# Optimization experiments

Hardware: AMD Instinct MI355X
Metric: run time of the kernel (lower is better)

The kernel has to match this reference:

```python
import jax, jax.numpy as jnp
import numpy as np

N = 50000       # num_node
E = 800000      # num edges (avg degree 32)
F_IN, F_HID, F_OUT = 128, 128, 64


def setup_inputs() -> dict:
    key = jax.random.key(0)
    ks = jax.random.split(key, 8)
    x = jax.random.normal(ks[0], (N, F_IN), dtype=jnp.float32)
    edge_index = jax.random.randint(ks[1], (2, E), 0, N, dtype=jnp.int64)
    edge_weight = jax.random.uniform(ks[2], (E,), dtype=jnp.float32)
    s1 = 1.0 / np.sqrt(F_IN)
    s2 = 1.0 / np.sqrt(F_HID)
    W1 = jax.random.normal(ks[3], (F_HID, F_IN), dtype=jnp.float32) * s1
    b1 = jnp.zeros((F_HID,), dtype=jnp.float32)
    W2 = jax.random.normal(ks[4], (F_HID, F_HID), dtype=jnp.float32) * s2
    b2 = jnp.zeros((F_HID,), dtype=jnp.float32)
    W3 = jax.random.normal(ks[5], (F_OUT, F_HID), dtype=jnp.float32) * s2
    b3 = jnp.zeros((F_OUT,), dtype=jnp.float32)
    return {"x": x, "edge_index": edge_index, "edge_weight": edge_weight,
            "W1": W1, "b1": b1, "W2": W2, "b2": b2, "W3": W3, "b3": b3}


def _gcn_norm(edge_index, edge_weight, num_nodes):
    # PyG gcn_norm: add self-loops (weight 1), symmetric D^-1/2 (A+I) D^-1/2
    loop = jnp.arange(num_nodes, dtype=edge_index.dtype)
    row = jnp.concatenate([edge_index[0], loop])  # source
    col = jnp.concatenate([edge_index[1], loop])  # target (aggregation index)
    ew = jnp.concatenate([edge_weight, jnp.ones((num_nodes,), edge_weight.dtype)])
    deg = jax.ops.segment_sum(ew, col, num_segments=num_nodes)
    deg_safe = jnp.where(deg > 0, deg, 1.0)
    dinv = jnp.where(deg > 0, jax.lax.rsqrt(deg_safe), 0.0)
    norm = dinv[row] * ew * dinv[col]  # [E+N]
    return row, col, norm


def reference(x, edge_index, edge_weight, W1, b1, W2, b2, W3, b3):
    num_nodes = x.shape[0]
    row, col, norm = _gcn_norm(edge_index, edge_weight, num_nodes)
    h = x
    for W, b in ((W1, b1), (W2, b2), (W3, b3)):
        m = h @ W.T                                   # [N, d_out]
        msg = m[row] * norm[:, None]                  # gather + scale, [E+N, d_out]
        agg = jax.ops.segment_sum(msg, col, num_segments=num_nodes)
        h = jax.nn.relu(agg + b)                      # GCNConv bias then ReLU
    return h.reshape(-1)                              # torch.flatten
```

## Files before the change

### kernel.cpp

```cpp
#include <hip/hip_runtime.h>
#include <hip/hip_fp16.h>


#define K_DIM 128
#define SORT_ITEMS 2048

typedef unsigned long long u64;
typedef unsigned int u32;

using half8   = __attribute__((ext_vector_type(8))) _Float16;
using floatx4 = __attribute__((ext_vector_type(4))) float;


__global__ void build_kernel(const int* __restrict__ row, const int* __restrict__ col,
                             const float* __restrict__ ew, u64* __restrict__ el,
                             int E, int N) {
    int i = blockIdx.x * blockDim.x + threadIdx.x;
    if (i < E) {
        el[i] = ((u64)(u32)col[i] << 48) | ((u64)(u32)row[i] << 32)
              | (u64)__float_as_uint(ew[i]);
    } else if (i < E + N) {
        int v = i - E;
        el[i] = ((u64)(u32)v << 48) | ((u64)(u32)v << 32)
              | (u64)__float_as_uint(1.0f);
    }
}

__global__ void p1_hist(const u64* __restrict__ el, u32* __restrict__ ghist,
                        int total, int nb) {
    __shared__ u32 bin[256];
    bin[threadIdx.x] = 0;
    __syncthreads();
    const int base = blockIdx.x * SORT_ITEMS;
    const int end = min(base + SORT_ITEMS, total);
    for (int i = base + threadIdx.x; i < end; i += 256)
        atomicAdd(&bin[(u32)(el[i] >> 56)], 1u);
    __syncthreads();
    ghist[(size_t)threadIdx.x * nb + blockIdx.x] = bin[threadIdx.x];
}

__global__ void digit_sum(const u32* __restrict__ ghist, u32* __restrict__ dsum, int nb) {
    __shared__ u32 s[256];
    const int d = blockIdx.x;
    u32 acc = 0;
    for (int i = threadIdx.x; i < nb; i += 256) acc += ghist[(size_t)d * nb + i];
    s[threadIdx.x] = acc;
    __syncthreads();
    for (int off = 128; off > 0; off >>= 1) {
        if (threadIdx.x < off) s[threadIdx.x] += s[threadIdx.x + off];
        __syncthreads();
    }
    if (threadIdx.x == 0) dsum[d] = s[0];
}

__global__ void dsum_scan(const u32* __restrict__ dsum, u32* __restrict__ dbase) {
    __shared__ u32 s[256];
    const int t = threadIdx.x;
    const u32 v = dsum[t];
    s[t] = v;
    __syncthreads();
    for (int off = 1; off < 256; off <<= 1) {
        u32 u = (t >= off) ? s[t - off] : 0;
        __syncthreads();
        s[t] += u;
        __syncthreads();
    }
    dbase[t] = s[t] - v;
    if (t == 255) dbase[256] = s[255];
}

__global__ void digit_scan(u32* __restrict__ ghist, const u32* __restrict__ dbase, int nb) {
    __shared__ u32 s[256];
    const int d = blockIdx.x, t = threadIdx.x;
    u32 carry = dbase[d];
    for (int base = 0; base < nb; base += 256) {
        const int i = base + t;
        const u32 v = (i < nb) ? ghist[(size_t)d * nb + i] : 0;
        s[t] = v;
        __syncthreads();
        for (int off = 1; off < 256; off <<= 1) {
            u32 u = (t >= off) ? s[t - off] : 0;
            __syncthreads();
            s[t] += u;
            __syncthreads();
        }
        if (i < nb) ghist[(size_t)d * nb + i] = carry + s[t] - v;
        carry += s[255];
        __syncthreads();
    }
}

__global__ void p1_scatter(const u64* __restrict__ el, const u32* __restrict__ ghist,
                           u64* __restrict__ out, int total, int nb) {
    __shared__ u32 cur[256];
    cur[threadIdx.x] = ghist[(size_t)threadIdx.x * nb + blockIdx.x];
    __syncthreads();
    const int base = blockIdx.x * SORT_ITEMS;
    const int end = min(base + SORT_ITEMS, total);
    for (int i = base + threadIdx.x; i < end; i += 256) {
        u64 e = el[i];
        u32 p = atomicAdd(&cur[(u32)(e >> 56)], 1u);
        out[p] = e;
    }
}

__global__ void p2_sort(const u64* __restrict__ in, u64* __restrict__ out,
                        const u32* __restrict__ dbase) {
    const int t = threadIdx.x;
    const int base = (int)dbase[blockIdx.x];
    const int size = (int)dbase[blockIdx.x + 1] - base;
    __shared__ u32 hist[256], cur[256], s[256];
    hist[t] = 0;
    __syncthreads();
    for (int i = t; i < size; i += 256)
        atomicAdd(&hist[(u32)(in[base + i] >> 48) & 0xFFu], 1u);
    __syncthreads();
    const u32 v = hist[t];
    s[t] = v;
    __syncthreads();
    for (int off = 1; off < 256; off <<= 1) {
        u32 u = (t >= off) ? s[t - off] : 0;
        __syncthreads();
        s[t] += u;
        __syncthreads();
    }
    cur[t] = (u32)base + s[t] - v;
    __syncthreads();
    for (int i = t; i < size; i += 256) {
        u64 e = in[base + i];
        u32 p = atomicAdd(&cur[(u32)(e >> 48) & 0xFFu], 1u);
        out[p] = e;
    }
}

__global__ void boundary_kernel(const u64* __restrict__ el, int* __restrict__ offs,
                                int total, int n) {
    int i = blockIdx.x * blockDim.x + threadIdx.x;
    if (i >= total) return;
    int c = (int)(el[i] >> 48);
    if (i == 0 || c != (int)(el[i - 1] >> 48)) offs[c] = i;
    if (i == 0) offs[n] = total;
}

__global__ void dinv_kernel(const u64* __restrict__ el, const int* __restrict__ offs,
                            float* __restrict__ dinv, int n) {
    int i = blockIdx.x * blockDim.x + threadIdx.x;
    if (i >= n) return;
    const int b = offs[i], e = offs[i + 1];
    float s = 0.f;
    for (int k = b; k < e; ++k)
        s += __uint_as_float((u32)(el[k] & 0xFFFFFFFFu));
    dinv[i] = rsqrtf(s);
}

__global__ void w2h_kernel(const float* __restrict__ W1, const float* __restrict__ W2,
                           const float* __restrict__ W3, __half* __restrict__ Wh,
                           int n1, int n2, int n3) {
    int i = blockIdx.x * blockDim.x + threadIdx.x;
    if (i >= n1 + n2 + n3) return;
    float v = (i < n1) ? W1[i] : (i < n1 + n2 ? W2[i - n1] : W3[i - n1 - n2]);
    Wh[i] = __float2half_rn(v);
}


template <int BN, bool FP32IN>
__global__ __launch_bounds__(256) void mfma_gemm(const void* __restrict__ Ain,
                                                 const __half* __restrict__ Wh,
                                                 const float* __restrict__ dinv,
                                                 __half* __restrict__ C, int nrows) {
    constexpr int NT = BN / 16;
    const int wave = threadIdx.x >> 6;
    const int lane = threadIdx.x & 63;
    const int quad = lane >> 4;
    const int l16  = lane & 15;
    const int row0 = blockIdx.x * 64 + wave * 16;

    int arow = row0 + l16;
    if (arow > nrows - 1) arow = nrows - 1;

    floatx4 acc[NT] = {};

#pragma unroll
    for (int kc = 0; kc < 4; ++kc) {
        const int kof = kc * 32 + quad * 8;
        half8 af;
        if constexpr (FP32IN) {
            const float* ap = (const float*)Ain + (size_t)arow * K_DIM + kof;
            float4 f0 = *(const float4*)ap;
            float4 f1 = *(const float4*)(ap + 4);
            af[0] = (_Float16)f0.x; af[1] = (_Float16)f0.y;
            af[2] = (_Float16)f0.z; af[3] = (_Float16)f0.w;
            af[4] = (_Float16)f1.x; af[5] = (_Float16)f1.y;
            af[6] = (_Float16)f1.z; af[7] = (_Float16)f1.w;
        } else {
            af = *(const half8*)((const __half*)Ain + (size_t)arow * K_DIM + kof);
        }
#pragma unroll
        for (int ct = 0; ct < NT; ++ct) {
            half8 bf = *(const half8*)(Wh + (size_t)(ct * 16 + l16) * K_DIM + kof);
            acc[ct] = __builtin_amdgcn_mfma_f32_16x16x32_f16(af, bf, acc[ct], 0, 0, 0);
        }
    }

    float dv[4];
    int grow[4];
    bool ok[4];
#pragma unroll
    for (int r = 0; r < 4; ++r) {
        grow[r] = row0 + quad * 4 + r;
        ok[r] = grow[r] < nrows;
        dv[r] = ok[r] ? dinv[grow[r]] : 0.f;
    }
#pragma unroll
    for (int ct = 0; ct < NT; ++ct) {
        const int colb = ct * 16 + l16;
#pragma unroll
        for (int r = 0; r < 4; ++r)
            if (ok[r])
                C[(size_t)grow[r] * BN + colb] = __float2half_rn(acc[ct][r] * dv[r]);
    }
}


template <int D, typename OUT>
__global__ __launch_bounds__(256) void agg_kernel(
    const __half* __restrict__ m, const int* __restrict__ offs,
    const int2* __restrict__ csr, const float* __restrict__ dinv,
    const float* __restrict__ bias, OUT* __restrict__ out, int n) {
    const int wid = threadIdx.x >> 6;
    const int lane = threadIdx.x & 63;
    const int node = (blockIdx.x << 2) + wid;
    if (node >= n) return;
    const int beg = offs[node];
    const int end = offs[node + 1];
    const __half2* mh = (const __half2*)m;
    float acc0 = 0.f, acc1 = 0.f;

    if constexpr (D == 128) {
        int k = beg;
        for (; k + 8 <= end; k += 8) {
            int2 e[8];
            float2 f[8];
#pragma unroll
            for (int j = 0; j < 8; ++j) e[j] = csr[k + j];
#pragma unroll
            for (int j = 0; j < 8; ++j)
                f[j] = __half22float2(mh[(size_t)(e[j].y & 0xFFFF) * 64 + lane]);
#pragma unroll
            for (int j = 0; j < 8; ++j) {
                float w = __int_as_float(e[j].x);
                acc0 = fmaf(w, f[j].x, acc0);
                acc1 = fmaf(w, f[j].y, acc1);
            }
        }
        for (; k < end; ++k) {
            int2 e0 = csr[k];
            float w0 = __int_as_float(e0.x);
            float2 f0 = __half22float2(mh[(size_t)(e0.y & 0xFFFF) * 64 + lane]);
            acc0 = fmaf(w0, f0.x, acc0); acc1 = fmaf(w0, f0.y, acc1);
        }
        const float dv = dinv[node];
        const float2 bv = *(const float2*)(bias + 2 * lane);
        float ox = fmaxf(acc0 * dv + bv.x, 0.f);
        float oy = fmaxf(acc1 * dv + bv.y, 0.f);
        if constexpr (sizeof(OUT) == 2) {
            ((__half2*)out)[(size_t)node * 64 + lane] = __floats2half2_rn(ox, oy);
        } else {
            *(float2*)((float*)out + (size_t)node * 128 + 2 * lane) = make_float2(ox, oy);
        }
    } else {
        const int half = lane >> 5;
        const int sl = lane & 31;
        int k = beg;
        for (; k + 8 <= end; k += 8) {
            int2 e0 = csr[k + half], e1 = csr[k + 2 + half];
            int2 e2 = csr[k + 4 + half], e3 = csr[k + 6 + half];
            float2 f0 = __half22float2(mh[(size_t)(e0.y & 0xFFFF) * 32 + sl]);
            float2 f1 = __half22float2(mh[(size_t)(e1.y & 0xFFFF) * 32 + sl]);
            float2 f2 = __half22float2(mh[(size_t)(e2.y & 0xFFFF) * 32 + sl]);
            float2 f3 = __half22float2(mh[(size_t)(e3.y & 0xFFFF) * 32 + sl]);
            float w0 = __int_as_float(e0.x), w1 = __int_as_float(e1.x);
            float w2 = __int_as_float(e2.x), w3 = __int_as_float(e3.x);
            acc0 = fmaf(w0, f0.x, acc0); acc1 = fmaf(w0, f0.y, acc1);
            acc0 = fmaf(w1, f1.x, acc0); acc1 = fmaf(w1, f1.y, acc1);
            acc0 = fmaf(w2, f2.x, acc0); acc1 = fmaf(w2, f2.y, acc1);
            acc0 = fmaf(w3, f3.x, acc0); acc1 = fmaf(w3, f3.y, acc1);
        }
        for (; k + 2 <= end; k += 2) {
            int2 e0 = csr[k + half];
            float w0 = __int_as_float(e0.x);
            float2 f0 = __half22float2(mh[(size_t)(e0.y & 0xFFFF) * 32 + sl]);
            acc0 = fmaf(w0, f0.x, acc0); acc1 = fmaf(w0, f0.y, acc1);
        }
        if (k < end && half == 0) {
            int2 e0 = csr[k];
            float w0 = __int_as_float(e0.x);
            float2 f0 = __half22float2(mh[(size_t)(e0.y & 0xFFFF) * 32 + sl]);
            acc0 = fmaf(w0, f0.x, acc0); acc1 = fmaf(w0, f0.y, acc1);
        }
        acc0 += __shfl_xor(acc0, 32);
        acc1 += __shfl_xor(acc1, 32);
        if (half == 0) {
            const float dv = dinv[node];
            const float2 bv = *(const float2*)(bias + 2 * sl);
            float ox = fmaxf(acc0 * dv + bv.x, 0.f);
            float oy = fmaxf(acc1 * dv + bv.y, 0.f);
            *(float2*)((float*)out + (size_t)node * 64 + 2 * sl) = make_float2(ox, oy);
        }
    }
}


extern "C" void kernel_launch(void* const* d_in, const int* in_sizes, int n_in,
                              void* d_out, int out_size, void* d_ws, size_t ws_size,
                              hipStream_t stream) {
    const float* x  = (const float*)d_in[0];
    const int*   ei = (const int*)d_in[1];
    const float* ew = (const float*)d_in[2];
    const float* W1 = (const float*)d_in[3];
    const float* b1 = (const float*)d_in[4];
    const float* W2 = (const float*)d_in[5];
    const float* b2 = (const float*)d_in[6];
    const float* W3 = (const float*)d_in[7];
    const float* b3 = (const float*)d_in[8];
    float* out = (float*)d_out;

    const int N = in_sizes[0] / K_DIM;
    const int E = in_sizes[2];
    const int* row = ei;
    const int* col = ei + E;

    const int total = E + N;
    const int nb = (total + SORT_ITEMS - 1) / SORT_ITEMS;
    const int ngroups = (N + 255) >> 8;
    const int NW1 = 128 * 128, NW2 = 128 * 128, NW3 = 64 * 128;

    u64* elA      = (u64*)d_ws;
    u64* elB      = elA + total;
    __half* m_buf = (__half*)(elB + total);
    __half* h_buf = m_buf + (size_t)N * K_DIM;
    __half* Wh    = h_buf + (size_t)N * K_DIM;
    u32* ghist    = (u32*)(Wh + NW1 + NW2 + NW3);
    u32* dsum     = ghist + (size_t)256 * nb;
    u32* dbase    = dsum + 256;
    int* offs     = (int*)(dbase + 257);
    float* dinv   = (float*)(offs + N + 1);

    build_kernel<<<(total + 255) / 256, 256, 0, stream>>>(row, col, ew, elA, E, N);
    p1_hist<<<nb, 256, 0, stream>>>(elA, ghist, total, nb);
    digit_sum<<<256, 256, 0, stream>>>(ghist, dsum, nb);
    dsum_scan<<<1, 256, 0, stream>>>(dsum, dbase);
    digit_scan<<<256, 256, 0, stream>>>(ghist, dbase, nb);
    p1_scatter<<<nb, 256, 0, stream>>>(elA, ghist, elB, total, nb);
    p2_sort<<<ngroups, 256, 0, stream>>>(elB, elA, dbase);
    boundary_kernel<<<(total + 255) / 256, 256, 0, stream>>>(elA, offs, total, N);
    dinv_kernel<<<(N + 255) / 256, 256, 0, stream>>>(elA, offs, dinv, N);
    w2h_kernel<<<(NW1 + NW2 + NW3 + 255) / 256, 256, 0, stream>>>(W1, W2, W3, Wh,
                                                                  NW1, NW2, NW3);

    const int gemm_blocks = (N + 63) / 64;
    const int agg_blocks = (N + 3) / 4;
    const int2* csr = (const int2*)elA;

    mfma_gemm<128, true><<<gemm_blocks, 256, 0, stream>>>(x, Wh, dinv, m_buf, N);
    agg_kernel<128, __half><<<agg_blocks, 256, 0, stream>>>(m_buf, offs, csr, dinv, b1, h_buf, N);
    mfma_gemm<128, false><<<gemm_blocks, 256, 0, stream>>>(h_buf, Wh + NW1, dinv, m_buf, N);
    agg_kernel<128, __half><<<agg_blocks, 256, 0, stream>>>(m_buf, offs, csr, dinv, b2, h_buf, N);
    mfma_gemm<64, false><<<gemm_blocks, 256, 0, stream>>>(h_buf, Wh + NW1 + NW2, dinv, m_buf, N);
    agg_kernel<64, float><<<agg_blocks, 256, 0, stream>>>(m_buf, offs, csr, dinv, b3, out, N);
}
```

Before: 313.4 us.

## Fuse CSR build preprocessing kernels to cut launches and global passes

Merges edge-list construction with the first radix histogram and folds the weight fp16 conversion into the same launch as extra blocks. The single-block digit-base scan is recomputed redundantly inside each digit_scan block. Segment offsets and degree rsqrt are now computed inside the second sort pass with shared-memory float atomics, removing the boundary and dinv kernels. This reduces kernel launches and extra reads of the sorted edge list. In exchange, the degree sums are accumulated in a nondeterministic order, and offsets are written only for nodes with nonzero count, which is always true here because of the self-loops.

```diff
diff --git a/kernel.cpp b/kernel.cpp
--- a/kernel.cpp
+++ b/kernel.cpp
@@ -12,31 +12,43 @@
 using floatx4 = __attribute__((ext_vector_type(4))) float;
 
 
-__global__ void build_kernel(const int* __restrict__ row, const int* __restrict__ col,
-                             const float* __restrict__ ew, u64* __restrict__ el,
-                             int E, int N) {
-    int i = blockIdx.x * blockDim.x + threadIdx.x;
-    if (i < E) {
-        el[i] = ((u64)(u32)col[i] << 48) | ((u64)(u32)row[i] << 32)
-              | (u64)__float_as_uint(ew[i]);
-    } else if (i < E + N) {
-        int v = i - E;
-        el[i] = ((u64)(u32)v << 48) | ((u64)(u32)v << 32)
-              | (u64)__float_as_uint(1.0f);
-    }
-}
-
-__global__ void p1_hist(const u64* __restrict__ el, u32* __restrict__ ghist,
-                        int total, int nb) {
+__global__ void build_hist(const int* __restrict__ row, const int* __restrict__ col,
+                           const float* __restrict__ ew, u64* __restrict__ el,
+                           u32* __restrict__ ghist, int E, int N, int nb,
+                           const float* __restrict__ W1, const float* __restrict__ W2,
+                           const float* __restrict__ W3, __half* __restrict__ Wh,
+                           int nw1, int nw2, int nw3) {
+    const int b = blockIdx.x;
+    if (b >= nb) {
+        const int i = (b - nb) * 256 + threadIdx.x;
+        const int tot = nw1 + nw2 + nw3;
+        if (i < tot) {
+            float v = (i < nw1) ? W1[i] : (i < nw1 + nw2 ? W2[i - nw1] : W3[i - nw1 - nw2]);
+            Wh[i] = __float2half_rn(v);
+        }
+        return;
+    }
     __shared__ u32 bin[256];
     bin[threadIdx.x] = 0;
     __syncthreads();
-    const int base = blockIdx.x * SORT_ITEMS;
+    const int total = E + N;
+    const int base = b * SORT_ITEMS;
     const int end = min(base + SORT_ITEMS, total);
-    for (int i = base + threadIdx.x; i < end; i += 256)
-        atomicAdd(&bin[(u32)(el[i] >> 56)], 1u);
-    __syncthreads();
-    ghist[(size_t)threadIdx.x * nb + blockIdx.x] = bin[threadIdx.x];
+    for (int i = base + threadIdx.x; i < end; i += 256) {
+        u64 e;
+        if (i < E) {
+            e = ((u64)(u32)col[i] << 48) | ((u64)(u32)row[i] << 32)
+              | (u64)__float_as_uint(ew[i]);
+        } else {
+            int v = i - E;
+            e = ((u64)(u32)v << 48) | ((u64)(u32)v << 32)
+              | (u64)__float_as_uint(1.0f);
+        }
+        el[i] = e;
+        atomicAdd(&bin[(u32)(e >> 56)], 1u);
+    }
+    __syncthreads();
+    ghist[(size_t)threadIdx.x * nb + b] = bin[threadIdx.x];
 }
 
 __global__ void digit_sum(const u32* __restrict__ ghist, u32* __restrict__ dsum, int nb) {
@@ -53,26 +65,22 @@
     if (threadIdx.x == 0) dsum[d] = s[0];
 }
 
-__global__ void dsum_scan(const u32* __restrict__ dsum, u32* __restrict__ dbase) {
-    __shared__ u32 s[256];
-    const int t = threadIdx.x;
-    const u32 v = dsum[t];
-    s[t] = v;
-    __syncthreads();
-    for (int off = 1; off < 256; off <<= 1) {
-        u32 u = (t >= off) ? s[t - off] : 0;
-        __syncthreads();
-        s[t] += u;
-        __syncthreads();
-    }
-    dbase[t] = s[t] - v;
-    if (t == 255) dbase[256] = s[255];
-}
-
-__global__ void digit_scan(u32* __restrict__ ghist, const u32* __restrict__ dbase, int nb) {
+__global__ void digit_scan(u32* __restrict__ ghist, const u32* __restrict__ dsum,
+                           u32* __restrict__ dbase, int nb) {
+    __shared__ u32 ds[256];
     __shared__ u32 s[256];
     const int d = blockIdx.x, t = threadIdx.x;
-    u32 carry = dbase[d];
+    ds[t] = dsum[t];
+    __syncthreads();
+    for (int off = 1; off < 256; off <<= 1) {
+        u32 u = (t >= off) ? ds[t - off] : 0;
+        __syncthreads();
+        ds[t] += u;
+        __syncthreads();
+    }
+    u32 carry = (d == 0) ? 0u : ds[d - 1];
+    if (t == 0) dbase[d] = carry;
+    if (d == 255 && t == 0) dbase[256] = ds[255];
     for (int base = 0; base < nb; base += 256) {
         const int i = base + t;
         const u32 v = (i < nb) ? ghist[(size_t)d * nb + i] : 0;
@@ -105,12 +113,15 @@
 }
 
 __global__ void p2_sort(const u64* __restrict__ in, u64* __restrict__ out,
-                        const u32* __restrict__ dbase) {
+                        const u32* __restrict__ dbase,
+                        int* __restrict__ offs, float* __restrict__ dinv, int n) {
     const int t = threadIdx.x;
     const int base = (int)dbase[blockIdx.x];
     const int size = (int)dbase[blockIdx.x + 1] - base;
     __shared__ u32 hist[256], cur[256], s[256];
+    __shared__ float wsum[256];
     hist[t] = 0;
+    wsum[t] = 0.f;
     __syncthreads();
     for (int i = t; i < size; i += 256)
         atomicAdd(&hist[(u32)(in[base + i] >> 48) & 0xFFu], 1u);
@@ -124,42 +135,23 @@
         s[t] += u;
         __syncthreads();
     }
-    cur[t] = (u32)base + s[t] - v;
+    const u32 mystart = (u32)base + s[t] - v;
+    cur[t] = mystart;
     __syncthreads();
     for (int i = t; i < size; i += 256) {
         u64 e = in[base + i];
-        u32 p = atomicAdd(&cur[(u32)(e >> 48) & 0xFFu], 1u);
+        u32 lo = (u32)(e >> 48) & 0xFFu;
+        u32 p = atomicAdd(&cur[lo], 1u);
         out[p] = e;
-    }
-}
-
-__global__ void boundary_kernel(const u64* __restrict__ el, int* __restrict__ offs,
-                                int total, int n) {
-    int i = blockIdx.x * blockDim.x + threadIdx.x;
-    if (i >= total) return;
-    int c = (int)(el[i] >> 48);
-    if (i == 0 || c != (int)(el[i - 1] >> 48)) offs[c] = i;
-    if (i == 0) offs[n] = total;
-}
-
-__global__ void dinv_kernel(const u64* __restrict__ el, const int* __restrict__ offs,
-                            float* __restrict__ dinv, int n) {
-    int i = blockIdx.x * blockDim.x + threadIdx.x;
-    if (i >= n) return;
-    const int b = offs[i], e = offs[i + 1];
-    float s = 0.f;
-    for (int k = b; k < e; ++k)
-        s += __uint_as_float((u32)(el[k] & 0xFFFFFFFFu));
-    dinv[i] = rsqrtf(s);
-}
-
-__global__ void w2h_kernel(const float* __restrict__ W1, const float* __restrict__ W2,
-                           const float* __restrict__ W3, __half* __restrict__ Wh,
-                           int n1, int n2, int n3) {
-    int i = blockIdx.x * blockDim.x + threadIdx.x;
-    if (i >= n1 + n2 + n3) return;
-    float v = (i < n1) ? W1[i] : (i < n1 + n2 ? W2[i - n1] : W3[i - n1 - n2]);
-    Wh[i] = __float2half_rn(v);
+        atomicAdd(&wsum[lo], __uint_as_float((u32)(e & 0xFFFFFFFFu)));
+    }
+    __syncthreads();
+    const int node = blockIdx.x * 256 + t;
+    if (node < n && v > 0) {
+        offs[node] = (int)mystart;
+        dinv[node] = rsqrtf(wsum[t]);
+        if (node == n - 1) offs[n] = (int)(mystart + v);
+    }
 }
 
 
@@ -334,6 +326,7 @@
     const int nb = (total + SORT_ITEMS - 1) / SORT_ITEMS;
     const int ngroups = (N + 255) >> 8;
     const int NW1 = 128 * 128, NW2 = 128 * 128, NW3 = 64 * 128;
+    const int nwb = (NW1 + NW2 + NW3 + 255) / 256;
 
     u64* elA      = (u64*)d_ws;
     u64* elB      = elA + total;
@@ -346,17 +339,12 @@
     int* offs     = (int*)(dbase + 257);
     float* dinv   = (float*)(offs + N + 1);
 
-    build_kernel<<<(total + 255) / 256, 256, 0, stream>>>(row, col, ew, elA, E, N);
-    p1_hist<<<nb, 256, 0, stream>>>(elA, ghist, total, nb);
+    build_hist<<<nb + nwb, 256, 0, stream>>>(row, col, ew, elA, ghist, E, N, nb,
+                                             W1, W2, W3, Wh, NW1, NW2, NW3);
     digit_sum<<<256, 256, 0, stream>>>(ghist, dsum, nb);
-    dsum_scan<<<1, 256, 0, stream>>>(dsum, dbase);
-    digit_scan<<<256, 256, 0, stream>>>(ghist, dbase, nb);
+    digit_scan<<<256, 256, 0, stream>>>(ghist, dsum, dbase, nb);
     p1_scatter<<<nb, 256, 0, stream>>>(elA, ghist, elB, total, nb);
-    p2_sort<<<ngroups, 256, 0, stream>>>(elB, elA, dbase);
-    boundary_kernel<<<(total + 255) / 256, 256, 0, stream>>>(elA, offs, total, N);
-    dinv_kernel<<<(N + 255) / 256, 256, 0, stream>>>(elA, offs, dinv, N);
-    w2h_kernel<<<(NW1 + NW2 + NW3 + 255) / 256, 256, 0, stream>>>(W1, W2, W3, Wh,
-                                                                  NW1, NW2, NW3);
+    p2_sort<<<ngroups, 256, 0, stream>>>(elB, elA, dbase, offs, dinv, N);
 
     const int gemm_blocks = (N + 63) / 64;
     const int agg_blocks = (N + 3) / 4;
```

After: 297.8 us. 5.0% less time.
